# Kernel optimization log

Hardware: AMD Instinct MI355X
Metric: run time of the kernel (lower is better)

Reference implementation:

```python
import jax, jax.numpy as jnp
import numpy as np

K_ORDER = 4
BETA = 0.5
NUM_HEADS = 1
IN_CHANNELS = 128


def _gcn_conv(x, row, col, values, N):
    # x: [N, H, D]; symmetric-normalized scatter-add message passing
    deg = jax.ops.segment_sum(values, row, num_segments=N)            # [N]
    dinv = jnp.where(deg > 0, deg ** -0.5, jnp.zeros_like(deg))
    coef = dinv[row] * dinv[col] * values                             # [E]
    return jax.ops.segment_sum(x[col] * coef[:, None, None], row, num_segments=N)


def _fast_attn_conv(qs, ks, vs, batch, pos, n_nodes_f, B, max_node):
    # qs/ks/vs: [N, H, D]; ragged graphs padded to [B, max_node, H, D]
    N, H, D = vs.shape
    q_pad = jnp.zeros((B, max_node, H, D), qs.dtype).at[batch, pos].set(qs)
    k_pad = jnp.zeros((B, max_node, H, D), ks.dtype).at[batch, pos].set(ks)
    v_pad = jnp.zeros((B, max_node, H, D), vs.dtype).at[batch, pos].set(vs)
    qk = jnp.einsum('bmhd,bnhd->bmhn', q_pad, k_pad)                  # [B, M, H, M]
    v_sum = jax.ops.segment_sum(vs, batch, num_segments=B)            # [B, H, D]
    numer_pad = jnp.einsum('bmhn,bnhd->bmhd', qk, v_pad)              # [B, M, H, D]
    numer = numer_pad[batch, pos] + v_sum[batch]                      # [N, H, D]
    denom = qk[batch, pos].sum(-1) + n_nodes_f[batch][:, None]        # [N, H]
    return numer / denom[..., None]


def _forward(x, edge_weight, Wq_w, Wq_b, Wk_w, Wk_b, Wo_w, Wo_b,
             row, col, batch, pos, n_nodes_f, B, max_node):
    N, C = x.shape
    H = NUM_HEADS
    query = (x @ Wq_w.T + Wq_b).reshape(N, H, C)
    key = (x @ Wk_w.T + Wk_b).reshape(N, H, C)
    qs = query / jnp.linalg.norm(query, axis=2, keepdims=True)
    ks = key / jnp.linalg.norm(key, axis=2, keepdims=True)
    cur = jnp.broadcast_to(x[:, None, :], (N, H, C))                  # x_0
    acc = cur
    for _ in range(K_ORDER):
        gcn_i = _gcn_conv(cur, row, col, edge_weight, N)
        attn_i = _fast_attn_conv(qs, ks, cur, batch, pos, n_nodes_f, B, max_node)
        cur = BETA * gcn_i + (1.0 - BETA) * attn_i
        acc = acc + cur
    out = acc.reshape(N, H * C) @ Wo_w.T + Wo_b
    return out / H


def setup_inputs():
    key = jax.random.key(0)
    k = jax.random.split(key, 10)
    B, per_graph = 64, 512
    N = B * per_graph
    C, H, OUT = IN_CHANNELS, NUM_HEADS, 128
    E = N * 16
    s = 1.0 / np.sqrt(C)
    return {
        'x': jax.random.normal(k[0], (N, C), jnp.float32),
        'edge_index': jax.random.randint(k[1], (2, E), 0, N, jnp.int32),
        'edge_weight': jax.random.uniform(k[2], (E,), jnp.float32),
        'n_nodes': jnp.full((B,), per_graph, jnp.int32),
        'Wq_w': jax.random.uniform(k[3], (H * C, C), jnp.float32, -s, s),
        'Wq_b': jax.random.uniform(k[4], (H * C,), jnp.float32, -s, s),
        'Wk_w': jax.random.uniform(k[5], (H * C, C), jnp.float32, -s, s),
        'Wk_b': jax.random.uniform(k[6], (H * C,), jnp.float32, -s, s),
        'Wo_w': jax.random.uniform(k[7], (OUT, H * C), jnp.float32, -s, s),
        'Wo_b': jax.random.uniform(k[8], (OUT,), jnp.float32, -s, s),
    }


def reference(x, edge_index, edge_weight, n_nodes, Wq_w, Wq_b, Wk_w, Wk_b, Wo_w, Wo_b):
    n_np = np.asarray(n_nodes)
    B, max_node = n_np.shape[0], int(n_np.max())
    N = x.shape[0]
    batch = jnp.asarray(np.repeat(np.arange(B), n_np))                # [N] graph id per node
    offsets = jnp.asarray(np.concatenate([[0], np.cumsum(n_np)[:-1]]))
    pos = jnp.arange(N) - offsets[batch]                              # within-graph index
    n_nodes_f = jnp.asarray(n_np, jnp.float32)
    row, col = edge_index[0], edge_index[1]
    return _forward(x, edge_weight, Wq_w, Wq_b, Wk_w, Wk_b, Wo_w, Wo_b,
                    row, col, batch, pos, n_nodes_f, B, max_node)
```

## Files before the change

### kernel.cpp

```cpp
#include <hip/hip_runtime.h>
#include <stdint.h>

#define C 128

typedef __attribute__((ext_vector_type(8))) short bfrag;
typedef __attribute__((ext_vector_type(4))) float ffrag;

__device__ __forceinline__ unsigned short f2bf(float f){
  union { float f; unsigned int i; } v; v.f = f;
  unsigned int x = v.i;
  unsigned int r = x + 0x7fffu + ((x >> 16) & 1u);
  return (unsigned short)(r >> 16);
}
__device__ __forceinline__ float bf2f(unsigned short u){
  union { unsigned int i; float f; } v; v.i = ((unsigned int)u) << 16; return v.f;
}

__global__ void k_zero_region(unsigned int* base, int nwords){
  int i = blockIdx.x * 256 + threadIdx.x;
  if (i < nwords) base[i] = 0u;
}

__global__ void k_degcast(const int* __restrict__ row, const float* __restrict__ w,
                          unsigned long long* deg64, int* __restrict__ rank, int E,
                          const float* __restrict__ Wq, const float* __restrict__ Wk,
                          const float* __restrict__ Wo, unsigned short* __restrict__ W16,
                          int WW, int degB){
  int bx = blockIdx.x;
  if (bx < degB){
    int e = bx * 256 + threadIdx.x;
    if (e < E){
      int r = row[e];
      unsigned int wf = (unsigned int)(w[e] * 16777216.0f + 0.5f);
      unsigned long long old =
          atomicAdd(&deg64[r], 0x100000000ULL | (unsigned long long)wf);
      rank[e] = (int)(old >> 32);
    }
  } else {
    int i = (bx - degB) * 256 + threadIdx.x;
    if (i < 3 * WW){
      const float* src = (i < WW) ? Wq : ((i < 2 * WW) ? Wk : Wo);
      int off = (i < WW) ? 0 : ((i < 2 * WW) ? WW : 2 * WW);
      W16[i] = f2bf(src[i - off]);
    }
  }
}

__global__ void k_scan1(const unsigned long long* __restrict__ deg64,
                        float* __restrict__ dinv, int* bsum, int N){
  __shared__ int s[256];
  int b = blockIdx.x, t = threadIdx.x;
  int i = b * 256 + t;
  int cnt = 0;
  if (i < N){
    unsigned long long v = deg64[i];
    cnt = (int)(v >> 32);
    unsigned int lo = (unsigned int)v;
    float d = (float)lo * (1.0f / 16777216.0f);
    dinv[i] = lo > 0u ? 1.0f / sqrtf(d) : 0.f;
  }
  s[t] = cnt;
  __syncthreads();
  for (int o = 128; o; o >>= 1){ if (t < o) s[t] += s[t + o]; __syncthreads(); }
  if (t == 0) bsum[b] = s[0];
}

__global__ void k_scan3(const unsigned long long* __restrict__ deg64,
                        const int* __restrict__ bsum, int* row_ptr, int N){
  __shared__ int s[256];
  int b = blockIdx.x, t = threadIdx.x;
  int i = b * 256 + t;
  int v = (i < N) ? (int)(deg64[i] >> 32) : 0;
  s[t] = v;
  __syncthreads();
  for (int o = 1; o < 256; o <<= 1){
    int u = (t >= o) ? s[t - o] : 0;
    __syncthreads(); s[t] += u; __syncthreads();
  }
  int base = 0;
  for (int j = 0; j < b; j++) base += bsum[j];
  int excl = base + s[t] - v;
  if (i < N) row_ptr[i] = excl;
  if (i == N - 1) row_ptr[N] = excl + v;
}

__global__ __launch_bounds__(256) void k_fillprep(
    const int* __restrict__ row, const int* __restrict__ col,
    const float* __restrict__ w, const int* __restrict__ rank,
    const int* __restrict__ row_ptr, const float* __restrict__ dinv,
    int2* __restrict__ edge_s, int E, int fillB,
    const float* __restrict__ x, unsigned short* __restrict__ cur16,
    unsigned short* __restrict__ curT, float* __restrict__ accf,
    float* __restrict__ vsum, int N, int PG){
  __shared__ unsigned short tile[64][66];
  __shared__ float ssum[4][64];
  int bx = blockIdx.x;
  if (bx < fillB){
    int e = bx * 256 + threadIdx.x;
    if (e < E){
      int r = row[e], c = col[e];
      int p = row_ptr[r] + rank[e];
      float cf = dinv[r] * dinv[c] * w[e];
      int2 ed; ed.x = c; ed.y = __float_as_int(cf);
      edge_s[p] = ed;
    }
    return;
  }
  int pb = bx - fillB;
  int ntiles = N >> 6;
  int n0 = (pb % ntiles) * 64;
  int c0 = (pb / ntiles) * 64;
  int tx = threadIdx.x & 63, ty = threadIdx.x >> 6;
  int b = n0 / PG;
  for (int r = ty; r < 64; r += 4){
    float v = x[(size_t)(n0 + r) * C + c0 + tx];
    accf[(size_t)(n0 + r) * C + c0 + tx] = v;
    unsigned short u = f2bf(v);
    cur16[(size_t)(n0 + r) * C + c0 + tx] = u;
    tile[r][tx] = u;
  }
  __syncthreads();
  for (int r = ty; r < 64; r += 4)
    curT[(size_t)(c0 + r) * N + n0 + tx] = tile[tx][r];
  float ps = 0.f;
  for (int r = ty * 16; r < ty * 16 + 16; r++) ps += bf2f(tile[r][tx]);
  ssum[ty][tx] = ps;
  __syncthreads();
  if (ty == 0){
    float s2 = ssum[0][tx] + ssum[1][tx] + ssum[2][tx] + ssum[3][tx];
    atomicAdd(&vsum[b * C + c0 + tx], s2);
  }
}

__global__ __launch_bounds__(256) void k_proj2(const unsigned short* __restrict__ x,
      const unsigned short* __restrict__ W16,
      const float* __restrict__ Wq_b, const float* __restrict__ Wk_b,
      unsigned short* __restrict__ qs, unsigned short* __restrict__ ksT,
      float* __restrict__ ksum, int N, int PG, int wblocks){
  int bx = blockIdx.x;
  int transposed = bx >= wblocks;
  int lb = transposed ? bx - wblocks : bx;
  const unsigned short* W = transposed ? (W16 + C * C) : W16;
  const float* Wb = transposed ? Wk_b : Wq_b;
  unsigned short* out = transposed ? ksT : qs;

  int wv = threadIdx.x >> 6, l = threadIdx.x & 63;
  int m0 = (lb * 4 + wv) * 16;
  if (m0 >= N) return;
  int quad = l >> 4, lcol = l & 15;
  ffrag acc[8] = {};
  const unsigned short* Abase = x + (size_t)(m0 + lcol) * C + quad * 8;
#pragma unroll
  for (int s = 0; s < 4; s++){
    bfrag a = *(const bfrag*)(Abase + s * 32);
#pragma unroll
    for (int nt = 0; nt < 8; nt++){
      bfrag bb = *(const bfrag*)(W + (size_t)(nt * 16 + lcol) * C + s * 32 + quad * 8);
      acc[nt] = __builtin_amdgcn_mfma_f32_16x16x32_bf16(a, bb, acc[nt], 0, 0, 0);
    }
  }
  float q[8][4];
  float ss[4] = {0.f, 0.f, 0.f, 0.f};
#pragma unroll
  for (int nt = 0; nt < 8; nt++){
    float bias = Wb[nt * 16 + lcol];
#pragma unroll
    for (int r = 0; r < 4; r++){ float v = acc[nt][r] + bias; q[nt][r] = v; ss[r] += v * v; }
  }
#pragma unroll
  for (int off = 1; off < 16; off <<= 1){
#pragma unroll
    for (int r = 0; r < 4; r++) ss[r] += __shfl_xor(ss[r], off, 64);
  }
  float inv[4];
#pragma unroll
  for (int r = 0; r < 4; r++) inv[r] = 1.0f / sqrtf(fmaxf(ss[r], 1e-30f));
  if (!transposed){
#pragma unroll
    for (int nt = 0; nt < 8; nt++)
#pragma unroll
      for (int r = 0; r < 4; r++)
        out[(size_t)(m0 + quad * 4 + r) * C + nt * 16 + lcol] = f2bf(q[nt][r] * inv[r]);
  } else {
    int b = m0 / PG;
#pragma unroll
    for (int nt = 0; nt < 8; nt++){
      ushort4 pk;
      float v0 = q[nt][0] * inv[0], v1 = q[nt][1] * inv[1];
      float v2 = q[nt][2] * inv[2], v3 = q[nt][3] * inv[3];
      pk.x = f2bf(v0); pk.y = f2bf(v1); pk.z = f2bf(v2); pk.w = f2bf(v3);
      *(ushort4*)(out + (size_t)(nt * 16 + lcol) * N + m0 + quad * 4) = pk;
      float s = v0 + v1 + v2 + v3;
      s += __shfl_xor(s, 16, 64);
      s += __shfl_xor(s, 32, 64);
      if (quad == 0) atomicAdd(&ksum[b * C + nt * 16 + lcol], s);
    }
  }
}

__global__ void k_denom(const unsigned short* __restrict__ qs, const float* __restrict__ ksum,
                        const int* __restrict__ n_nodes, float* denom, int N, int PG){
  int wv = threadIdx.x >> 6, l = threadIdx.x & 63;
  int m = blockIdx.x * 4 + wv;
  if (m >= N) return;
  int b = m / PG;
  float s = bf2f(qs[(size_t)m * C + l]) * ksum[b * C + l]
          + bf2f(qs[(size_t)m * C + 64 + l]) * ksum[b * C + 64 + l];
#pragma unroll
  for (int off = 32; off; off >>= 1) s += __shfl_xor(s, off, 64);
  if (l == 0) denom[m] = s + (float)n_nodes[b];
}

__global__ __launch_bounds__(256) void k_mid(const unsigned short* __restrict__ ksT,
      const unsigned short* __restrict__ curT, unsigned short* __restrict__ MT,
      const int* __restrict__ row_ptr, const int2* __restrict__ edge_s,
      const unsigned int* __restrict__ cur32, unsigned int* __restrict__ gcn32,
      float* __restrict__ vsumN, int N, int PG, int BC, int mB, int gcnB){
  int bx = blockIdx.x;
  if (bx < mB){
    int wv = threadIdx.x >> 6, l = threadIdx.x & 63;
    int b = bx >> 2;
    int gw = (bx & 3) * 4 + wv;
    int itile = gw & 7, jh = gw >> 3;
    int quad = l >> 4, lcol = l & 15;
    ffrag acc[4] = {};
    const unsigned short* Arow = ksT + (size_t)(itile * 16 + lcol) * N + (size_t)b * PG + quad * 8;
    const unsigned short* B0 = curT + (size_t)b * PG + quad * 8;
    int steps = PG / 32;
    for (int s = 0; s < steps; s++){
      bfrag a = *(const bfrag*)(Arow + s * 32);
#pragma unroll
      for (int jt = 0; jt < 4; jt++){
        bfrag bb = *(const bfrag*)(B0 + (size_t)((jh * 4 + jt) * 16 + lcol) * N + s * 32);
        acc[jt] = __builtin_amdgcn_mfma_f32_16x16x32_bf16(a, bb, acc[jt], 0, 0, 0);
      }
    }
    unsigned short* MTb = MT + (size_t)b * C * C;
    int i0 = itile * 16 + quad * 4;
#pragma unroll
    for (int jt = 0; jt < 4; jt++){
      int j = (jh * 4 + jt) * 16 + lcol;
      ushort4 pk;
      pk.x = f2bf(acc[jt][0]); pk.y = f2bf(acc[jt][1]);
      pk.z = f2bf(acc[jt][2]); pk.w = f2bf(acc[jt][3]);
      *(ushort4*)(MTb + (size_t)j * C + i0) = pk;
    }
    return;
  }
  bx -= mB;
  if (bx < gcnB){
    int nid = bx * 4 + (threadIdx.x >> 6);
    int c = threadIdx.x & 63;
    if (nid >= N) return;
    int s = row_ptr[nid], e = row_ptr[nid + 1];
    float a0 = 0.f, a1 = 0.f;
    int p = s;
    for (; p + 4 <= e; p += 4){
      int2 e0 = edge_s[p],     e1 = edge_s[p + 1];
      int2 e2 = edge_s[p + 2], e3 = edge_s[p + 3];
      float f0 = __int_as_float(e0.y), f1 = __int_as_float(e1.y);
      float f2 = __int_as_float(e2.y), f3 = __int_as_float(e3.y);
      unsigned int u0 = cur32[(size_t)e0.x * 64 + c];
      unsigned int u1 = cur32[(size_t)e1.x * 64 + c];
      unsigned int u2 = cur32[(size_t)e2.x * 64 + c];
      unsigned int u3 = cur32[(size_t)e3.x * 64 + c];
      a0 += f0 * bf2f((unsigned short)(u0 & 0xffffu));
      a1 += f0 * bf2f((unsigned short)(u0 >> 16));
      a0 += f1 * bf2f((unsigned short)(u1 & 0xffffu));
      a1 += f1 * bf2f((unsigned short)(u1 >> 16));
      a0 += f2 * bf2f((unsigned short)(u2 & 0xffffu));
      a1 += f2 * bf2f((unsigned short)(u2 >> 16));
      a0 += f3 * bf2f((unsigned short)(u3 & 0xffffu));
      a1 += f3 * bf2f((unsigned short)(u3 >> 16));
    }
    for (; p < e; p++){
      int2 ed = edge_s[p];
      float cf = __int_as_float(ed.y);
      unsigned int u = cur32[(size_t)ed.x * 64 + c];
      a0 += cf * bf2f((unsigned short)(u & 0xffffu));
      a1 += cf * bf2f((unsigned short)(u >> 16));
    }
    gcn32[(size_t)nid * 64 + c] = ((unsigned int)f2bf(a1) << 16) | (unsigned int)f2bf(a0);
    return;
  }
  bx -= gcnB;
  if (vsumN){
    int idx = bx * 256 + threadIdx.x;
    if (idx < BC) vsumN[idx] = 0.f;
  }
}

__global__ __launch_bounds__(256) void k_phase2(const unsigned short* __restrict__ qs,
      const unsigned short* __restrict__ MT, const float* __restrict__ vsum,
      const float* __restrict__ denom, const unsigned short* __restrict__ gcn16,
      unsigned short* __restrict__ cur16, unsigned short* __restrict__ curT,
      float* __restrict__ accf, unsigned short* __restrict__ acc16,
      float* __restrict__ vsumN,
      int N, int PG, int last){
  int wv = threadIdx.x >> 6, l = threadIdx.x & 63;
  int m0 = (blockIdx.x * 4 + wv) * 16;
  if (m0 >= N) return;
  int b = m0 / PG;
  int quad = l >> 4, lcol = l & 15;
  ffrag acc[8] = {};
  const unsigned short* Abase = qs + (size_t)(m0 + lcol) * C + quad * 8;
  const unsigned short* MTb = MT + (size_t)b * C * C;
#pragma unroll
  for (int s = 0; s < 4; s++){
    bfrag a = *(const bfrag*)(Abase + s * 32);
#pragma unroll
    for (int dt = 0; dt < 8; dt++){
      bfrag bb = *(const bfrag*)(MTb + (size_t)(dt * 16 + lcol) * C + s * 32 + quad * 8);
      acc[dt] = __builtin_amdgcn_mfma_f32_16x16x32_bf16(a, bb, acc[dt], 0, 0, 0);
    }
  }
  float dn[4];
#pragma unroll
  for (int r = 0; r < 4; r++) dn[r] = denom[m0 + quad * 4 + r];
#pragma unroll
  for (int dt = 0; dt < 8; dt++){
    int d = dt * 16 + lcol;
    float vs = vsum[b * C + d];
    ushort4 pk;
    float vnext = 0.f;
#pragma unroll
    for (int r = 0; r < 4; r++){
      int m = m0 + quad * 4 + r;
      float attn = (acc[dt][r] + vs) / dn[r];
      float g = bf2f(gcn16[(size_t)m * C + d]);
      float nc = 0.5f * (g + attn);
      float na = accf[(size_t)m * C + d] + nc;
      accf[(size_t)m * C + d] = na;
      unsigned short nb = f2bf(nc);
      cur16[(size_t)m * C + d] = nb;
      if (last) acc16[(size_t)m * C + d] = f2bf(na);
      ((unsigned short*)&pk)[r] = nb;
      vnext += bf2f(nb);
    }
    *(ushort4*)(curT + (size_t)d * N + m0 + quad * 4) = pk;
    if (vsumN){
      vnext += __shfl_xor(vnext, 16, 64);
      vnext += __shfl_xor(vnext, 32, 64);
      if (quad == 0) atomicAdd(&vsumN[b * C + d], vnext);
    }
  }
}

__global__ __launch_bounds__(256) void k_final(const unsigned short* __restrict__ acc16,
      const unsigned short* __restrict__ Wo, const float* __restrict__ Wob,
      float* __restrict__ out, int N){
  int wv = threadIdx.x >> 6, l = threadIdx.x & 63;
  int m0 = (blockIdx.x * 4 + wv) * 16;
  if (m0 >= N) return;
  int quad = l >> 4, lcol = l & 15;
  ffrag acc[8] = {};
  const unsigned short* Abase = acc16 + (size_t)(m0 + lcol) * C + quad * 8;
#pragma unroll
  for (int s = 0; s < 4; s++){
    bfrag a = *(const bfrag*)(Abase + s * 32);
#pragma unroll
    for (int ot = 0; ot < 8; ot++){
      bfrag bb = *(const bfrag*)(Wo + (size_t)(ot * 16 + lcol) * C + s * 32 + quad * 8);
      acc[ot] = __builtin_amdgcn_mfma_f32_16x16x32_bf16(a, bb, acc[ot], 0, 0, 0);
    }
  }
#pragma unroll
  for (int ot = 0; ot < 8; ot++){
    float bias = Wob[ot * 16 + lcol];
#pragma unroll
    for (int r = 0; r < 4; r++){
      out[(size_t)(m0 + quad * 4 + r) * C + ot * 16 + lcol] = acc[ot][r] + bias;
    }
  }
}


extern "C" void kernel_launch(void* const* d_in, const int* in_sizes, int n_in,
                              void* d_out, int out_size, void* d_ws, size_t ws_size,
                              hipStream_t stream){
  const float* x    = (const float*)d_in[0];
  const int*   eidx = (const int*)d_in[1];
  const float* ew   = (const float*)d_in[2];
  const int*   n_nodes = (const int*)d_in[3];
  const float* Wq_w = (const float*)d_in[4];
  const float* Wq_b = (const float*)d_in[5];
  const float* Wk_w = (const float*)d_in[6];
  const float* Wk_b = (const float*)d_in[7];
  const float* Wo_w = (const float*)d_in[8];
  const float* Wo_b = (const float*)d_in[9];
  float* out = (float*)d_out;

  int N = in_sizes[0] / C;
  int E = in_sizes[2];
  int B = in_sizes[3];
  int PG = N / B;
  int BC = B * C;
  const int* row = eidx;
  const int* col = eidx + E;

  char* p = (char*)d_ws;
  auto alloc = [&](size_t bytes) -> void* {
    void* r = (void*)p; p += (bytes + 255) & ~(size_t)255; return r;
  };
  unsigned short* cur16 = (unsigned short*)alloc((size_t)N * C * 2);
  unsigned short* curT  = (unsigned short*)alloc((size_t)N * C * 2);
  unsigned short* qs16  = (unsigned short*)alloc((size_t)N * C * 2);
  unsigned short* ksT   = (unsigned short*)alloc((size_t)N * C * 2);
  unsigned short* gcn16 = (unsigned short*)alloc((size_t)N * C * 2);
  unsigned short* acc16 = (unsigned short*)alloc((size_t)N * C * 2);
  float*          accf  = (float*)alloc((size_t)N * C * 4);
  unsigned short* MT    = (unsigned short*)alloc((size_t)B * C * C * 2);
  unsigned short* W16   = (unsigned short*)alloc((size_t)3 * C * C * 2);
  char* zbase = (char*)alloc((size_t)N * 8 + (size_t)BC * 8);
  unsigned long long* deg64 = (unsigned long long*)zbase;
  float*          ksum  = (float*)(zbase + (size_t)N * 8);
  float*          vsumA = (float*)(zbase + (size_t)N * 8 + (size_t)BC * 4);
  float*          dinv  = (float*)alloc((size_t)N * 4);
  int*            row_ptr = (int*)alloc((size_t)(N + 1) * 4);
  int*            rank  = (int*)alloc((size_t)E * 4);
  int*            bsum  = (int*)alloc(1024);
  int2*           edge_s = (int2*)alloc((size_t)E * 8);
  float*          vsumB = (float*)alloc((size_t)BC * 4);
  float*          denom = (float*)alloc((size_t)N * 4);

  dim3 b256(256);
  int wblocks = (N / 16 + 3) / 4;
  int WW = C * C;
  int nscan = (N + 255) / 256;
  int degB = (E + 255) / 256;
  int castB = (3 * WW + 255) / 256;
  int fillB = (E + 255) / 256;
  int prepB = (N / 64) * (C / 64);
  int mB = 4 * B;
  int gcnB = (N + 3) / 4;
  int zvB = (BC + 255) / 256;
  int zwords = 2 * N + 2 * BC;

  k_zero_region<<<dim3((zwords + 255) / 256), b256, 0, stream>>>((unsigned int*)deg64, zwords);
  k_degcast<<<dim3(degB + castB), b256, 0, stream>>>(row, ew, deg64, rank, E,
                                                     Wq_w, Wk_w, Wo_w, W16, WW, degB);
  k_scan1<<<dim3(nscan), b256, 0, stream>>>(deg64, dinv, bsum, N);
  k_scan3<<<dim3(nscan), b256, 0, stream>>>(deg64, bsum, row_ptr, N);
  k_fillprep<<<dim3(fillB + prepB), b256, 0, stream>>>(row, col, ew, rank, row_ptr, dinv,
                                                       edge_s, E, fillB,
                                                       x, cur16, curT, accf, vsumA, N, PG);
  k_proj2<<<dim3(2 * wblocks), b256, 0, stream>>>(cur16, W16, Wq_b, Wk_b,
                                                  qs16, ksT, ksum, N, PG, wblocks);
  k_denom<<<dim3((N + 3) / 4), b256, 0, stream>>>(qs16, ksum, n_nodes, denom, N, PG);

  float* vs_cur = vsumA;
  float* vs_nxt = vsumB;
  for (int it = 0; it < 4; it++){
    int last = (it == 3);
    k_mid<<<dim3(mB + gcnB + zvB), b256, 0, stream>>>(ksT, curT, MT, row_ptr, edge_s,
                                                      (const unsigned int*)cur16,
                                                      (unsigned int*)gcn16,
                                                      last ? (float*)nullptr : vs_nxt,
                                                      N, PG, BC, mB, gcnB);
    k_phase2<<<dim3(wblocks), b256, 0, stream>>>(qs16, MT, vs_cur, denom, gcn16,
                                                 cur16, curT, accf, acc16,
                                                 last ? (float*)nullptr : vs_nxt,
                                                 N, PG, last);
    float* tmp = vs_cur; vs_cur = vs_nxt; vs_nxt = tmp;
  }

  k_final<<<dim3(wblocks), b256, 0, stream>>>(acc16, W16 + 2 * WW, Wo_b, out, N);
}
```

Before: 416.8 us.

## Replace atomic column sums and fp32 accumulator with deterministic reductions and buffered iterates

Drops the running fp32 accumulator (read-modify-write of N×C floats every iteration) and instead keeps each iterate in its own bf16 buffer, summing x and the four iterates inside the final projection kernel. Per-graph value and key sums, previously built with atomicAdd in the prep, projection and phase2 kernels, are now computed by dedicated reduction blocks in k_mid from the transposed buffers, which also removes the zeroing passes. This cuts per-iteration global traffic and atomic contention, at the cost of extra reads from the transposed arrays and more workspace memory. Because denom depends on ksum, k_denom moves to after the first k_mid launch.

```diff
diff --git a/kernel.cpp b/kernel.cpp
--- a/kernel.cpp
+++ b/kernel.cpp
@@ -89,11 +89,9 @@
     const float* __restrict__ w, const int* __restrict__ rank,
     const int* __restrict__ row_ptr, const float* __restrict__ dinv,
     int2* __restrict__ edge_s, int E, int fillB,
-    const float* __restrict__ x, unsigned short* __restrict__ cur16,
-    unsigned short* __restrict__ curT, float* __restrict__ accf,
-    float* __restrict__ vsum, int N, int PG){
+    const float* __restrict__ x, unsigned short* __restrict__ cur0,
+    unsigned short* __restrict__ curT, int N){
   __shared__ unsigned short tile[64][66];
-  __shared__ float ssum[4][64];
   int bx = blockIdx.x;
   if (bx < fillB){
     int e = bx * 256 + threadIdx.x;
@@ -111,32 +109,22 @@
   int n0 = (pb % ntiles) * 64;
   int c0 = (pb / ntiles) * 64;
   int tx = threadIdx.x & 63, ty = threadIdx.x >> 6;
-  int b = n0 / PG;
   for (int r = ty; r < 64; r += 4){
     float v = x[(size_t)(n0 + r) * C + c0 + tx];
-    accf[(size_t)(n0 + r) * C + c0 + tx] = v;
     unsigned short u = f2bf(v);
-    cur16[(size_t)(n0 + r) * C + c0 + tx] = u;
+    cur0[(size_t)(n0 + r) * C + c0 + tx] = u;
     tile[r][tx] = u;
   }
   __syncthreads();
   for (int r = ty; r < 64; r += 4)
     curT[(size_t)(c0 + r) * N + n0 + tx] = tile[tx][r];
-  float ps = 0.f;
-  for (int r = ty * 16; r < ty * 16 + 16; r++) ps += bf2f(tile[r][tx]);
-  ssum[ty][tx] = ps;
-  __syncthreads();
-  if (ty == 0){
-    float s2 = ssum[0][tx] + ssum[1][tx] + ssum[2][tx] + ssum[3][tx];
-    atomicAdd(&vsum[b * C + c0 + tx], s2);
-  }
 }
 
 __global__ __launch_bounds__(256) void k_proj2(const unsigned short* __restrict__ x,
       const unsigned short* __restrict__ W16,
       const float* __restrict__ Wq_b, const float* __restrict__ Wk_b,
       unsigned short* __restrict__ qs, unsigned short* __restrict__ ksT,
-      float* __restrict__ ksum, int N, int PG, int wblocks){
+      int N, int wblocks){
   int bx = blockIdx.x;
   int transposed = bx >= wblocks;
   int lb = transposed ? bx - wblocks : bx;
@@ -182,18 +170,12 @@
       for (int r = 0; r < 4; r++)
         out[(size_t)(m0 + quad * 4 + r) * C + nt * 16 + lcol] = f2bf(q[nt][r] * inv[r]);
   } else {
-    int b = m0 / PG;
 #pragma unroll
     for (int nt = 0; nt < 8; nt++){
       ushort4 pk;
-      float v0 = q[nt][0] * inv[0], v1 = q[nt][1] * inv[1];
-      float v2 = q[nt][2] * inv[2], v3 = q[nt][3] * inv[3];
-      pk.x = f2bf(v0); pk.y = f2bf(v1); pk.z = f2bf(v2); pk.w = f2bf(v3);
+      pk.x = f2bf(q[nt][0] * inv[0]); pk.y = f2bf(q[nt][1] * inv[1]);
+      pk.z = f2bf(q[nt][2] * inv[2]); pk.w = f2bf(q[nt][3] * inv[3]);
       *(ushort4*)(out + (size_t)(nt * 16 + lcol) * N + m0 + quad * 4) = pk;
-      float s = v0 + v1 + v2 + v3;
-      s += __shfl_xor(s, 16, 64);
-      s += __shfl_xor(s, 32, 64);
-      if (quad == 0) atomicAdd(&ksum[b * C + nt * 16 + lcol], s);
     }
   }
 }
@@ -215,7 +197,8 @@
       const unsigned short* __restrict__ curT, unsigned short* __restrict__ MT,
       const int* __restrict__ row_ptr, const int2* __restrict__ edge_s,
       const unsigned int* __restrict__ cur32, unsigned int* __restrict__ gcn32,
-      float* __restrict__ vsumN, int N, int PG, int BC, int mB, int gcnB){
+      float* __restrict__ vsum, float* __restrict__ ksum,
+      int N, int PG, int mB, int vsB, int ksB, int gcnB){
   int bx = blockIdx.x;
   if (bx < mB){
     int wv = threadIdx.x >> 6, l = threadIdx.x & 63;
@@ -248,6 +231,25 @@
     return;
   }
   bx -= mB;
+  if (bx < vsB + ksB){
+    const unsigned short* src = (bx < vsB) ? curT : ksT;
+    float* dst = (bx < vsB) ? vsum : ksum;
+    int b = (bx < vsB) ? bx : (bx - vsB);
+    int wv = threadIdx.x >> 6, l = threadIdx.x & 63;
+    for (int d = wv * 32; d < wv * 32 + 32; d++){
+      float s = 0.f;
+      for (int n0 = l * 8; n0 < PG; n0 += 512){
+        bfrag v = *(const bfrag*)(src + (size_t)d * N + (size_t)b * PG + n0);
+#pragma unroll
+        for (int j = 0; j < 8; j++) s += bf2f((unsigned short)v[j]);
+      }
+#pragma unroll
+      for (int off = 32; off; off >>= 1) s += __shfl_xor(s, off, 64);
+      if (l == 0) dst[b * C + d] = s;
+    }
+    return;
+  }
+  bx -= vsB + ksB;
   if (bx < gcnB){
     int nid = bx * 4 + (threadIdx.x >> 6);
     int c = threadIdx.x & 63;
@@ -281,22 +283,14 @@
       a1 += cf * bf2f((unsigned short)(u >> 16));
     }
     gcn32[(size_t)nid * 64 + c] = ((unsigned int)f2bf(a1) << 16) | (unsigned int)f2bf(a0);
-    return;
-  }
-  bx -= gcnB;
-  if (vsumN){
-    int idx = bx * 256 + threadIdx.x;
-    if (idx < BC) vsumN[idx] = 0.f;
   }
 }
 
 __global__ __launch_bounds__(256) void k_phase2(const unsigned short* __restrict__ qs,
       const unsigned short* __restrict__ MT, const float* __restrict__ vsum,
       const float* __restrict__ denom, const unsigned short* __restrict__ gcn16,
-      unsigned short* __restrict__ cur16, unsigned short* __restrict__ curT,
-      float* __restrict__ accf, unsigned short* __restrict__ acc16,
-      float* __restrict__ vsumN,
-      int N, int PG, int last){
+      unsigned short* __restrict__ curO, unsigned short* __restrict__ curT,
+      int N, int PG){
   int wv = threadIdx.x >> 6, l = threadIdx.x & 63;
   int m0 = (blockIdx.x * 4 + wv) * 16;
   if (m0 >= N) return;
@@ -322,31 +316,22 @@
     int d = dt * 16 + lcol;
     float vs = vsum[b * C + d];
     ushort4 pk;
-    float vnext = 0.f;
 #pragma unroll
     for (int r = 0; r < 4; r++){
       int m = m0 + quad * 4 + r;
       float attn = (acc[dt][r] + vs) / dn[r];
       float g = bf2f(gcn16[(size_t)m * C + d]);
-      float nc = 0.5f * (g + attn);
-      float na = accf[(size_t)m * C + d] + nc;
-      accf[(size_t)m * C + d] = na;
-      unsigned short nb = f2bf(nc);
-      cur16[(size_t)m * C + d] = nb;
-      if (last) acc16[(size_t)m * C + d] = f2bf(na);
+      unsigned short nb = f2bf(0.5f * (g + attn));
+      curO[(size_t)m * C + d] = nb;
       ((unsigned short*)&pk)[r] = nb;
-      vnext += bf2f(nb);
     }
     *(ushort4*)(curT + (size_t)d * N + m0 + quad * 4) = pk;
-    if (vsumN){
-      vnext += __shfl_xor(vnext, 16, 64);
-      vnext += __shfl_xor(vnext, 32, 64);
-      if (quad == 0) atomicAdd(&vsumN[b * C + d], vnext);
-    }
-  }
-}
-
-__global__ __launch_bounds__(256) void k_final(const unsigned short* __restrict__ acc16,
+  }
+}
+
+__global__ __launch_bounds__(256) void k_final(const float* __restrict__ x,
+      const unsigned short* __restrict__ c1, const unsigned short* __restrict__ c2,
+      const unsigned short* __restrict__ c3, const unsigned short* __restrict__ c4,
       const unsigned short* __restrict__ Wo, const float* __restrict__ Wob,
       float* __restrict__ out, int N){
   int wv = threadIdx.x >> 6, l = threadIdx.x & 63;
@@ -354,10 +339,24 @@
   if (m0 >= N) return;
   int quad = l >> 4, lcol = l & 15;
   ffrag acc[8] = {};
-  const unsigned short* Abase = acc16 + (size_t)(m0 + lcol) * C + quad * 8;
+  size_t rowoff = (size_t)(m0 + lcol) * C + quad * 8;
 #pragma unroll
   for (int s = 0; s < 4; s++){
-    bfrag a = *(const bfrag*)(Abase + s * 32);
+    size_t base = rowoff + s * 32;
+    float4 xa0 = *(const float4*)(x + base);
+    float4 xa1 = *(const float4*)(x + base + 4);
+    bfrag b1 = *(const bfrag*)(c1 + base);
+    bfrag b2 = *(const bfrag*)(c2 + base);
+    bfrag b3 = *(const bfrag*)(c3 + base);
+    bfrag b4 = *(const bfrag*)(c4 + base);
+    float xs[8] = {xa0.x, xa0.y, xa0.z, xa0.w, xa1.x, xa1.y, xa1.z, xa1.w};
+    bfrag a;
+#pragma unroll
+    for (int j = 0; j < 8; j++){
+      float v = (((xs[j] + bf2f((unsigned short)b1[j])) + bf2f((unsigned short)b2[j]))
+                 + bf2f((unsigned short)b3[j])) + bf2f((unsigned short)b4[j]);
+      a[j] = (short)f2bf(v);
+    }
 #pragma unroll
     for (int ot = 0; ot < 8; ot++){
       bfrag bb = *(const bfrag*)(Wo + (size_t)(ot * 16 + lcol) * C + s * 32 + quad * 8);
@@ -402,25 +401,22 @@
   auto alloc = [&](size_t bytes) -> void* {
     void* r = (void*)p; p += (bytes + 255) & ~(size_t)255; return r;
   };
-  unsigned short* cur16 = (unsigned short*)alloc((size_t)N * C * 2);
+  unsigned short* cur[5];
+  for (int i = 0; i < 5; i++) cur[i] = (unsigned short*)alloc((size_t)N * C * 2);
   unsigned short* curT  = (unsigned short*)alloc((size_t)N * C * 2);
   unsigned short* qs16  = (unsigned short*)alloc((size_t)N * C * 2);
   unsigned short* ksT   = (unsigned short*)alloc((size_t)N * C * 2);
   unsigned short* gcn16 = (unsigned short*)alloc((size_t)N * C * 2);
-  unsigned short* acc16 = (unsigned short*)alloc((size_t)N * C * 2);
-  float*          accf  = (float*)alloc((size_t)N * C * 4);
   unsigned short* MT    = (unsigned short*)alloc((size_t)B * C * C * 2);
   unsigned short* W16   = (unsigned short*)alloc((size_t)3 * C * C * 2);
-  char* zbase = (char*)alloc((size_t)N * 8 + (size_t)BC * 8);
-  unsigned long long* deg64 = (unsigned long long*)zbase;
-  float*          ksum  = (float*)(zbase + (size_t)N * 8);
-  float*          vsumA = (float*)(zbase + (size_t)N * 8 + (size_t)BC * 4);
+  unsigned long long* deg64 = (unsigned long long*)alloc((size_t)N * 8);
   float*          dinv  = (float*)alloc((size_t)N * 4);
   int*            row_ptr = (int*)alloc((size_t)(N + 1) * 4);
   int*            rank  = (int*)alloc((size_t)E * 4);
   int*            bsum  = (int*)alloc(1024);
   int2*           edge_s = (int2*)alloc((size_t)E * 8);
-  float*          vsumB = (float*)alloc((size_t)BC * 4);
+  float*          ksum  = (float*)alloc((size_t)BC * 4);
+  float*          vsum  = (float*)alloc((size_t)BC * 4);
   float*          denom = (float*)alloc((size_t)N * 4);
 
   dim3 b256(256);
@@ -433,36 +429,32 @@
   int prepB = (N / 64) * (C / 64);
   int mB = 4 * B;
   int gcnB = (N + 3) / 4;
-  int zvB = (BC + 255) / 256;
-  int zwords = 2 * N + 2 * BC;
-
-  k_zero_region<<<dim3((zwords + 255) / 256), b256, 0, stream>>>((unsigned int*)deg64, zwords);
+  int vsB = B;
+
+  k_zero_region<<<dim3((2 * N + 255) / 256), b256, 0, stream>>>((unsigned int*)deg64, 2 * N);
   k_degcast<<<dim3(degB + castB), b256, 0, stream>>>(row, ew, deg64, rank, E,
                                                      Wq_w, Wk_w, Wo_w, W16, WW, degB);
   k_scan1<<<dim3(nscan), b256, 0, stream>>>(deg64, dinv, bsum, N);
   k_scan3<<<dim3(nscan), b256, 0, stream>>>(deg64, bsum, row_ptr, N);
   k_fillprep<<<dim3(fillB + prepB), b256, 0, stream>>>(row, col, ew, rank, row_ptr, dinv,
                                                        edge_s, E, fillB,
-                                                       x, cur16, curT, accf, vsumA, N, PG);
-  k_proj2<<<dim3(2 * wblocks), b256, 0, stream>>>(cur16, W16, Wq_b, Wk_b,
-                                                  qs16, ksT, ksum, N, PG, wblocks);
-  k_denom<<<dim3((N + 3) / 4), b256, 0, stream>>>(qs16, ksum, n_nodes, denom, N, PG);
-
-  float* vs_cur = vsumA;
-  float* vs_nxt = vsumB;
+                                                       x, cur[0], curT, N);
+  k_proj2<<<dim3(2 * wblocks), b256, 0, stream>>>(cur[0], W16, Wq_b, Wk_b,
+                                                  qs16, ksT, N, wblocks);
+
   for (int it = 0; it < 4; it++){
-    int last = (it == 3);
-    k_mid<<<dim3(mB + gcnB + zvB), b256, 0, stream>>>(ksT, curT, MT, row_ptr, edge_s,
-                                                      (const unsigned int*)cur16,
+    int ksB = (it == 0) ? B : 0;
+    k_mid<<<dim3(mB + vsB + ksB + gcnB), b256, 0, stream>>>(ksT, curT, MT, row_ptr, edge_s,
+                                                      (const unsigned int*)cur[it],
                                                       (unsigned int*)gcn16,
-                                                      last ? (float*)nullptr : vs_nxt,
-                                                      N, PG, BC, mB, gcnB);
-    k_phase2<<<dim3(wblocks), b256, 0, stream>>>(qs16, MT, vs_cur, denom, gcn16,
-                                                 cur16, curT, accf, acc16,
-                                                 last ? (float*)nullptr : vs_nxt,
-                                                 N, PG, last);
-    float* tmp = vs_cur; vs_cur = vs_nxt; vs_nxt = tmp;
-  }
-
-  k_final<<<dim3(wblocks), b256, 0, stream>>>(acc16, W16 + 2 * WW, Wo_b, out, N);
-}
+                                                      vsum, ksum,
+                                                      N, PG, mB, vsB, ksB, gcnB);
+    if (it == 0)
+      k_denom<<<dim3((N + 3) / 4), b256, 0, stream>>>(qs16, ksum, n_nodes, denom, N, PG);
+    k_phase2<<<dim3(wblocks), b256, 0, stream>>>(qs16, MT, vsum, denom, gcn16,
+                                                 cur[it + 1], curT, N, PG);
+  }
+
+  k_final<<<dim3(wblocks), b256, 0, stream>>>(x, cur[1], cur[2], cur[3], cur[4],
+                                              W16 + 2 * WW, Wo_b, out, N);
+}
```

Result: faster. 386.0 us (-7.4%).
